# Kernel tuning notes

Measured on AMD Instinct MI355X. Metric: run time of the kernel, lower is better.

## Reference

```python
import jax, jax.numpy as jnp
import numpy as np

N_NODES = 50000
N_EDGES = 800000
IN_DIM = 128
HID = 64
HEADS = 4
OUT = 16
N_GRAPHS = 500
NEG_SLOPE = 0.2


def setup_inputs() -> dict:
    key = jax.random.key(0)
    ks = jax.random.split(key, 12)
    x = jax.random.normal(ks[0], (N_NODES, IN_DIM), dtype=jnp.float32)
    edge_index = jax.random.randint(ks[1], (2, N_EDGES), 0, N_NODES, dtype=jnp.int64)
    batch = jnp.sort(jax.random.randint(ks[2], (N_NODES,), 0, N_GRAPHS, dtype=jnp.int64))
    s1 = 1.0 / np.sqrt(IN_DIM)
    s2 = 1.0 / np.sqrt(HID)
    W1 = jax.random.normal(ks[3], (IN_DIM, HEADS * HID), dtype=jnp.float32) * s1
    a1_src = jax.random.normal(ks[4], (HEADS, HID), dtype=jnp.float32) * s2
    a1_dst = jax.random.normal(ks[5], (HEADS, HID), dtype=jnp.float32) * s2
    b1 = jnp.zeros((HID,), dtype=jnp.float32)
    W2 = jax.random.normal(ks[6], (HID, HEADS * HID), dtype=jnp.float32) * s2
    a2_src = jax.random.normal(ks[7], (HEADS, HID), dtype=jnp.float32) * s2
    a2_dst = jax.random.normal(ks[8], (HEADS, HID), dtype=jnp.float32) * s2
    b2 = jnp.zeros((HID,), dtype=jnp.float32)
    fcW = jax.random.normal(ks[9], (HID, OUT), dtype=jnp.float32) * s2
    fcb = jnp.zeros((OUT,), dtype=jnp.float32)
    return {"x": x, "edge_index": edge_index, "batch": batch,
            "W1": W1, "a1_src": a1_src, "a1_dst": a1_dst, "b1": b1,
            "W2": W2, "a2_src": a2_src, "a2_dst": a2_dst, "b2": b2,
            "fcW": fcW, "fcb": fcb}


def gat_conv(x, W, a_src, a_dst, b, src, dst):
    # PyG GATConv with concat=False: per-head linear, edge softmax over dst, head-mean.
    n = x.shape[0]
    h = (x @ W).reshape(n, HEADS, HID)          # [N,H,D]
    alpha_s = jnp.sum(h * a_src, axis=-1)        # [N,H]
    alpha_d = jnp.sum(h * a_dst, axis=-1)        # [N,H]
    e = jax.nn.leaky_relu(alpha_s[src] + alpha_d[dst], NEG_SLOPE)  # [E,H]
    emax = jax.ops.segment_max(e, dst, num_segments=n)
    ex = jnp.exp(e - emax[dst])
    denom = jax.ops.segment_sum(ex, dst, num_segments=n)
    alpha = ex / denom[dst]                      # [E,H], edge softmax per dst
    msg = h[src] * alpha[:, :, None]             # [E,H,D]
    out = jax.ops.segment_sum(msg, dst, num_segments=n)  # [N,H,D]
    return out.mean(axis=1) + b                  # concat=False -> head mean


def reference(x, edge_index, batch, W1, a1_src, a1_dst, b1, W2, a2_src, a2_dst, b2, fcW, fcb):
    n = x.shape[0]
    # PyG GATConv default add_self_loops=True
    loops = jnp.arange(n, dtype=edge_index.dtype)
    src = jnp.concatenate([edge_index[0], loops])
    dst = jnp.concatenate([edge_index[1], loops])
    h = jax.nn.relu(gat_conv(x, W1, a1_src, a1_dst, b1, src, dst))
    h = jax.nn.relu(gat_conv(h, W2, a2_src, a2_dst, b2, src, dst))
    # global_mean_pool over batch ids
    sums = jax.ops.segment_sum(h, batch, num_segments=N_GRAPHS)
    counts = jax.ops.segment_sum(jnp.ones((n,), dtype=h.dtype), batch, num_segments=N_GRAPHS)
    pooled = sums / jnp.clip(counts, 1.0)[:, None]
    return pooled @ fcW + fcb
```

## Files before the change

### kernel.cpp

```cpp
#include <hip/hip_runtime.h>
#include <hip/hip_bf16.h>
#include <hip/hip_fp16.h>

#define NN 50000
#define EE 800000
#define ETOT 850000
#define NG 500
#define NBLK ((NN + 255) / 256)
#define EB ((ETOT + 255) / 256)

typedef __attribute__((ext_vector_type(8))) short bf16x8;
typedef __attribute__((ext_vector_type(4))) float f32x4;
typedef _Float16 h2f __attribute__((ext_vector_type(2)));

__device__ __forceinline__ h2f as_h2(unsigned u) {
    union { unsigned u; h2f h; } x;
    x.u = u;
    return x.h;
}

__device__ __forceinline__ unsigned short bf16_rne(float v) {
    unsigned u = __float_as_uint(v);
    unsigned r = u + 0x7FFFu + ((u >> 16) & 1u);
    return (unsigned short)(r >> 16);
}

__device__ __forceinline__ int detect_stride(const int* __restrict__ ei,
                                             int tid, int* sflag) {
    if (tid < 64) {
        unsigned long long b = __ballot(ei[2 * tid + 1] != 0);
        if (tid == 0) *sflag = b ? 1 : 2;
    }
    __syncthreads();
    return *sflag;
}

__device__ __forceinline__ void prepw_one(const float* __restrict__ W,
                                          const float* __restrict__ asrc,
                                          const float* __restrict__ adst,
                                          unsigned short* __restrict__ bhi,
                                          unsigned short* __restrict__ blo,
                                          float* __restrict__ ap,
                                          float* __restrict__ adp,
                                          int K, int t) {
    int j = t / K, k = t - j * K;
    int d = j >> 2, h = j & 3;
    float v = W[k * 256 + h * 64 + d];
    unsigned short hb = bf16_rne(v);
    float hf = __uint_as_float((unsigned)hb << 16);
    bhi[t] = hb;
    blo[t] = bf16_rne(v - hf);
    if (k == 0) { ap[j] = asrc[h * 64 + d]; adp[j] = adst[h * 64 + d]; }
}

__global__ __launch_bounds__(256) void k_prep(
        const int* __restrict__ ei, int* __restrict__ src32,
        int* __restrict__ dst32, int* __restrict__ deg,
        const float* __restrict__ W1, const float* __restrict__ a1s,
        const float* __restrict__ a1d, const float* __restrict__ W2,
        const float* __restrict__ a2s, const float* __restrict__ a2d,
        unsigned short* __restrict__ b1h, unsigned short* __restrict__ b1l,
        unsigned short* __restrict__ b2h, unsigned short* __restrict__ b2l,
        float* __restrict__ ap1, float* __restrict__ adp1,
        float* __restrict__ ap2, float* __restrict__ adp2) {
    int blk = blockIdx.x;
    if (blk >= EB) {
        int g = blk - EB;
        if (g < 128)
            prepw_one(W1, a1s, a1d, b1h, b1l, ap1, adp1, 128, g * 256 + threadIdx.x);
        else
            prepw_one(W2, a2s, a2d, b2h, b2l, ap2, adp2, 64, (g - 128) * 256 + threadIdx.x);
        return;
    }
    __shared__ int sflag;
    int tid = threadIdx.x;
    int st = detect_stride(ei, tid, &sflag);
    int e = blk * 256 + tid;
    if (e >= ETOT) return;
    int s, d;
    if (e < EE) {
        s = ei[(size_t)st * e];
        d = ei[(size_t)st * (EE + e)];
    } else {
        s = d = e - EE;
    }
    src32[e] = s;
    dst32[e] = d;
    atomicAdd(&deg[d], 1);
}

__global__ __launch_bounds__(256) void k_blocksum(const int* __restrict__ deg,
                                                  int* __restrict__ bsum) {
    __shared__ int l[256];
    int gid = blockIdx.x * 256 + threadIdx.x;
    int tid = threadIdx.x;
    l[tid] = (gid < NN) ? deg[gid] : 0;
    __syncthreads();
    for (int o = 128; o > 0; o >>= 1) {
        if (tid < o) l[tid] += l[tid + o];
        __syncthreads();
    }
    if (tid == 0) bsum[blockIdx.x] = l[0];
}

__global__ __launch_bounds__(256) void k_scan_final(const int* __restrict__ deg,
                                                    const int* __restrict__ bsum,
                                                    int* __restrict__ rowptr,
                                                    int* __restrict__ cursor) {
    __shared__ int lb[256];
    __shared__ int l[256];
    int tid = threadIdx.x;
    int vb = (tid < NBLK) ? bsum[tid] : 0;
    lb[tid] = vb;
    __syncthreads();
    for (int d = 1; d < 256; d <<= 1) {
        int t = (tid >= d) ? lb[tid - d] : 0;
        __syncthreads();
        lb[tid] += t;
        __syncthreads();
    }
    int boffb = lb[blockIdx.x] - bsum[blockIdx.x];
    int gid = blockIdx.x * 256 + tid;
    int v = (gid < NN) ? deg[gid] : 0;
    l[tid] = v;
    __syncthreads();
    for (int d = 1; d < 256; d <<= 1) {
        int t = (tid >= d) ? l[tid - d] : 0;
        __syncthreads();
        l[tid] += t;
        __syncthreads();
    }
    int ex = l[tid] - v + boffb;
    if (gid < NN) { rowptr[gid] = ex; cursor[gid] = ex; }
    if (gid == 0) rowptr[NN] = ETOT;
}

__global__ __launch_bounds__(256) void k_scatter(const int* __restrict__ src32,
                                                 const int* __restrict__ dst32,
                                                 int* __restrict__ cursor,
                                                 int* __restrict__ csr_src) {
    int e = blockIdx.x * 256 + threadIdx.x;
    if (e >= ETOT) return;
    int pos = atomicAdd(&cursor[dst32[e]], 1);
    csr_src[pos] = src32[e];
}

template <int K>
__global__ __launch_bounds__(64) void k_gemm_mfma(
        const float* __restrict__ A,
        const unsigned short* __restrict__ Bhi,
        const unsigned short* __restrict__ Blo,
        const float* __restrict__ aperm,
        const float* __restrict__ adperm,
        __half* __restrict__ C16,
        float* __restrict__ os,
        float* __restrict__ od, int M) {
    const int NC = K / 32;
    int lane = threadIdx.x;
    int l = lane & 15, q = lane >> 4;
    int m0 = blockIdx.x * 32;

    bf16x8 ahi[2][NC], alo[2][NC];
#pragma unroll
    for (int t = 0; t < 2; ++t) {
        int row = m0 + t * 16 + l;
        if (row >= M) row = M - 1;
        const float* arow = A + (size_t)row * K + q * 8;
#pragma unroll
        for (int c = 0; c < NC; ++c) {
            float4 v0 = *(const float4*)(arow + c * 32);
            float4 v1 = *(const float4*)(arow + c * 32 + 4);
            float vv[8] = {v0.x, v0.y, v0.z, v0.w, v1.x, v1.y, v1.z, v1.w};
#pragma unroll
            for (int j = 0; j < 8; ++j) {
                unsigned short hb = bf16_rne(vv[j]);
                float hf = __uint_as_float((unsigned)hb << 16);
                ahi[t][c][j] = (short)hb;
                alo[t][c][j] = (short)bf16_rne(vv[j] - hf);
            }
        }
    }

    float ps[2][4] = {}, pd[2][4] = {};
    const size_t brow = (size_t)l * K + q * 8;
#pragma unroll 2
    for (int n = 0; n < 16; ++n) {
        const unsigned short* bh = Bhi + (size_t)(n * 16) * K + brow;
        const unsigned short* bl = Blo + (size_t)(n * 16) * K + brow;
        bf16x8 bhf[NC], blf[NC];
#pragma unroll
        for (int c = 0; c < NC; ++c) {
            bhf[c] = *(const bf16x8*)(bh + c * 32);
            blf[c] = *(const bf16x8*)(bl + c * 32);
        }
        f32x4 acc0 = {0.f, 0.f, 0.f, 0.f}, acc1 = {0.f, 0.f, 0.f, 0.f};
#pragma unroll
        for (int c = 0; c < NC; ++c) {
            acc0 = __builtin_amdgcn_mfma_f32_16x16x32_bf16(ahi[0][c], bhf[c], acc0, 0, 0, 0);
            acc1 = __builtin_amdgcn_mfma_f32_16x16x32_bf16(ahi[1][c], bhf[c], acc1, 0, 0, 0);
            acc0 = __builtin_amdgcn_mfma_f32_16x16x32_bf16(ahi[0][c], blf[c], acc0, 0, 0, 0);
            acc1 = __builtin_amdgcn_mfma_f32_16x16x32_bf16(ahi[1][c], blf[c], acc1, 0, 0, 0);
            acc0 = __builtin_amdgcn_mfma_f32_16x16x32_bf16(alo[0][c], bhf[c], acc0, 0, 0, 0);
            acc1 = __builtin_amdgcn_mfma_f32_16x16x32_bf16(alo[1][c], bhf[c], acc1, 0, 0, 0);
        }
        float av = aperm[n * 16 + l], dv = adperm[n * 16 + l];
#pragma unroll
        for (int r = 0; r < 4; ++r) {
            ps[0][r] += acc0[r] * av; pd[0][r] += acc0[r] * dv;
            ps[1][r] += acc1[r] * av; pd[1][r] += acc1[r] * dv;
            int gm0 = m0 + q * 4 + r;
            if (gm0 < M) C16[(size_t)gm0 * 256 + n * 16 + l] = __float2half(acc0[r]);
            int gm1 = m0 + 16 + q * 4 + r;
            if (gm1 < M) C16[(size_t)gm1 * 256 + n * 16 + l] = __float2half(acc1[r]);
        }
    }
#pragma unroll
    for (int t = 0; t < 2; ++t)
#pragma unroll
        for (int r = 0; r < 4; ++r) {
            ps[t][r] += __shfl_xor(ps[t][r], 4);
            ps[t][r] += __shfl_xor(ps[t][r], 8);
            pd[t][r] += __shfl_xor(pd[t][r], 4);
            pd[t][r] += __shfl_xor(pd[t][r], 8);
        }
    if (l < 4) {
#pragma unroll
        for (int t = 0; t < 2; ++t)
#pragma unroll
            for (int r = 0; r < 4; ++r) {
                int gm = m0 + t * 16 + q * 4 + r;
                if (gm < M) {
                    os[(size_t)gm * 4 + l] = ps[t][r];
                    od[(size_t)gm * 4 + l] = pd[t][r];
                }
            }
    }
}

__device__ __forceinline__ float lrelu_exp(float x) {
    x = x > 0.f ? x : 0.2f * x;
    return __expf(x);
}

__global__ __launch_bounds__(256) void k_aggr(const int* __restrict__ rowptr,
                                              const int* __restrict__ csr_src,
                                              const float* __restrict__ as_,
                                              const float* __restrict__ ad_,
                                              const __half* __restrict__ h16,
                                              const float* __restrict__ bias,
                                              float* __restrict__ out) {
    __shared__ uint2 als16[4][64];
    __shared__ int sss[4][64];
    int w = threadIdx.x >> 6;
    int lane = threadIdx.x & 63;
    int d = blockIdx.x * 4 + w;
    if (d >= NN) return;
    int beg = rowptr[d], end = rowptr[d + 1];
    float4 adv = *(const float4*)(ad_ + d * 4);

    int s0 = 0;
    float4 u0 = make_float4(0.f, 0.f, 0.f, 0.f);
    float4 den = make_float4(0.f, 0.f, 0.f, 0.f);
    int i0 = beg + lane;
    if (i0 < end) {
        s0 = csr_src[i0];
        float4 sv = *(const float4*)(as_ + s0 * 4);
        u0.x = lrelu_exp(sv.x + adv.x);
        u0.y = lrelu_exp(sv.y + adv.y);
        u0.z = lrelu_exp(sv.z + adv.z);
        u0.w = lrelu_exp(sv.w + adv.w);
        den = u0;
    }
    for (int i = i0 + 64; i < end; i += 64) {
        int s = csr_src[i];
        float4 sv = *(const float4*)(as_ + s * 4);
        den.x += lrelu_exp(sv.x + adv.x);
        den.y += lrelu_exp(sv.y + adv.y);
        den.z += lrelu_exp(sv.z + adv.z);
        den.w += lrelu_exp(sv.w + adv.w);
    }
#pragma unroll
    for (int off = 32; off > 0; off >>= 1) {
        den.x += __shfl_xor(den.x, off);
        den.y += __shfl_xor(den.y, off);
        den.z += __shfl_xor(den.z, off);
        den.w += __shfl_xor(den.w, off);
    }
    float4 dinv = make_float4(0.25f / den.x, 0.25f / den.y,
                              0.25f / den.z, 0.25f / den.w);
    {
        __half2 q0 = __floats2half2_rn(u0.x * dinv.x, u0.y * dinv.y);
        __half2 q1 = __floats2half2_rn(u0.z * dinv.z, u0.w * dinv.w);
        als16[w][lane] = make_uint2(*(unsigned*)&q0, *(unsigned*)&q1);
        sss[w][lane] = s0;
    }

    int cnt = end - beg;
    if (cnt > 64) cnt = 64;
    int cnt4 = (cnt + 3) & ~3;
    float acc = 0.f;
    int4 sq = *(const int4*)&sss[w][0];
    uint2 r0 = *(const uint2*)(h16 + (size_t)sq.x * 256 + lane * 4);
    uint2 r1 = *(const uint2*)(h16 + (size_t)sq.y * 256 + lane * 4);
    uint2 r2 = *(const uint2*)(h16 + (size_t)sq.z * 256 + lane * 4);
    uint2 r3 = *(const uint2*)(h16 + (size_t)sq.w * 256 + lane * 4);
    for (int j = 0; j < cnt4; j += 4) {
        int jn = (j + 4) & 63;
        int4 sn = *(const int4*)&sss[w][jn];
        uint2 n0 = *(const uint2*)(h16 + (size_t)sn.x * 256 + lane * 4);
        uint2 n1 = *(const uint2*)(h16 + (size_t)sn.y * 256 + lane * 4);
        uint2 n2 = *(const uint2*)(h16 + (size_t)sn.z * 256 + lane * 4);
        uint2 n3 = *(const uint2*)(h16 + (size_t)sn.w * 256 + lane * 4);
        uint4 A01 = *(const uint4*)&als16[w][j];
        uint4 A23 = *(const uint4*)&als16[w][j + 2];
        acc = __builtin_amdgcn_fdot2(as_h2(r0.x), as_h2(A01.x), acc, false);
        acc = __builtin_amdgcn_fdot2(as_h2(r0.y), as_h2(A01.y), acc, false);
        acc = __builtin_amdgcn_fdot2(as_h2(r1.x), as_h2(A01.z), acc, false);
        acc = __builtin_amdgcn_fdot2(as_h2(r1.y), as_h2(A01.w), acc, false);
        acc = __builtin_amdgcn_fdot2(as_h2(r2.x), as_h2(A23.x), acc, false);
        acc = __builtin_amdgcn_fdot2(as_h2(r2.y), as_h2(A23.y), acc, false);
        acc = __builtin_amdgcn_fdot2(as_h2(r3.x), as_h2(A23.z), acc, false);
        acc = __builtin_amdgcn_fdot2(as_h2(r3.y), as_h2(A23.w), acc, false);
        r0 = n0; r1 = n1; r2 = n2; r3 = n3;
    }
    for (int chunk = beg + 64; chunk < end; chunk += 64) {
        int i = chunk + lane;
        int s = 0;
        float4 al = make_float4(0.f, 0.f, 0.f, 0.f);
        if (i < end) {
            s = csr_src[i];
            float4 sv = *(const float4*)(as_ + s * 4);
            al.x = lrelu_exp(sv.x + adv.x) * dinv.x;
            al.y = lrelu_exp(sv.y + adv.y) * dinv.y;
            al.z = lrelu_exp(sv.z + adv.z) * dinv.z;
            al.w = lrelu_exp(sv.w + adv.w) * dinv.w;
        }
        int cc = end - chunk;
        if (cc > 64) cc = 64;
        for (int j = 0; j < cc; ++j) {
            int sj = __shfl(s, j);
            float a0 = __shfl(al.x, j), a1 = __shfl(al.y, j);
            float a2 = __shfl(al.z, j), a3 = __shfl(al.w, j);
            uint2 raw = *(const uint2*)(h16 + (size_t)sj * 256 + lane * 4);
            float2 fa = __half22float2(*(const __half2*)&raw.x);
            float2 fb = __half22float2(*(const __half2*)&raw.y);
            acc += a0 * fa.x + a1 * fa.y + a2 * fb.x + a3 * fb.y;
        }
    }
    float v = acc + bias[lane];
    out[d * 64 + lane] = v > 0.f ? v : 0.f;
}

__global__ __launch_bounds__(256) void k_pool_fc(const float* __restrict__ x3,
                                                 const int* __restrict__ batch,
                                                 const int* __restrict__ ei,
                                                 const float* __restrict__ fcW,
                                                 const float* __restrict__ fcb,
                                                 float* __restrict__ out) {
    __shared__ int sflag;
    int tid = threadIdx.x, lane = tid & 63, w = tid >> 6;
    int st = detect_stride(ei, tid, &sflag);
    int g = blockIdx.x;
    int lo = 0, hi = NN;
    while (lo < hi) { int mid = (lo + hi) >> 1; if (batch[(size_t)st * mid] < g) lo = mid + 1; else hi = mid; }
    int start = lo;
    hi = NN;
    while (lo < hi) { int mid = (lo + hi) >> 1; if (batch[(size_t)st * mid] < g + 1) lo = mid + 1; else hi = mid; }
    int end = lo;
    float sum = 0.f;
    for (int n = start + w; n < end; n += 4) sum += x3[n * 64 + lane];
    __shared__ float ls[4][64];
    ls[w][lane] = sum;
    __syncthreads();
    if (w == 0) {
        float c = (float)(end - start);
        if (c < 1.f) c = 1.f;
        float p = (ls[0][lane] + ls[1][lane] + ls[2][lane] + ls[3][lane]) / c;
#pragma unroll
        for (int o = 0; o < 16; ++o) {
            float v = p * fcW[lane * 16 + o];
#pragma unroll
            for (int off = 32; off > 0; off >>= 1) v += __shfl_down(v, off);
            if (lane == 0) out[g * 16 + o] = v + fcb[o];
        }
    }
}

extern "C" void kernel_launch(void* const* d_in, const int* in_sizes, int n_in,
                              void* d_out, int out_size, void* d_ws, size_t ws_size,
                              hipStream_t stream) {
    const float* x   = (const float*)d_in[0];
    const int*   ei  = (const int*)d_in[1];
    const int*   bat = (const int*)d_in[2];
    const float* W1  = (const float*)d_in[3];
    const float* a1s = (const float*)d_in[4];
    const float* a1d = (const float*)d_in[5];
    const float* b1  = (const float*)d_in[6];
    const float* W2  = (const float*)d_in[7];
    const float* a2s = (const float*)d_in[8];
    const float* a2d = (const float*)d_in[9];
    const float* b2  = (const float*)d_in[10];
    const float* fcW = (const float*)d_in[11];
    const float* fcb = (const float*)d_in[12];
    float* out = (float*)d_out;

    float* ws = (float*)d_ws;
    __half* h16  = (__half*)(ws + 256);
    float* as_   = (float*)(h16 + (size_t)NN * 256);
    float* ad_   = as_ + NN * 4;
    float* xacc  = ad_ + NN * 4;
    int* src32   = (int*)(xacc + (size_t)NN * 64);
    int* dst32   = src32 + ETOT;
    int* deg     = dst32 + ETOT;
    int* rowptr  = deg + NN;
    int* cursor  = rowptr + NN + 1;
    int* csr_src = cursor + NN;
    int* bsum    = csr_src + ETOT;
    char* p = (char*)(bsum + NBLK);
    p = (char*)(((size_t)p + 255) & ~(size_t)255);
    unsigned short* bt1h = (unsigned short*)p; p += 256 * 128 * 2;
    unsigned short* bt1l = (unsigned short*)p; p += 256 * 128 * 2;
    unsigned short* bt2h = (unsigned short*)p; p += 256 * 64 * 2;
    unsigned short* bt2l = (unsigned short*)p; p += 256 * 64 * 2;
    float* ap1  = (float*)p; p += 256 * 4;
    float* adp1 = (float*)p; p += 256 * 4;
    float* ap2  = (float*)p; p += 256 * 4;
    float* adp2 = (float*)p; p += 256 * 4;

    const int wb = (NN * 64 + 255) / 256;

    hipMemsetAsync(deg, 0, NN * sizeof(int), stream);
    k_prep<<<EB + 192, 256, 0, stream>>>(ei, src32, dst32, deg,
                                         W1, a1s, a1d, W2, a2s, a2d,
                                         bt1h, bt1l, bt2h, bt2l,
                                         ap1, adp1, ap2, adp2);
    k_blocksum<<<NBLK, 256, 0, stream>>>(deg, bsum);
    k_scan_final<<<NBLK, 256, 0, stream>>>(deg, bsum, rowptr, cursor);
    k_scatter<<<EB, 256, 0, stream>>>(src32, dst32, cursor, csr_src);

    const int gg = (NN + 31) / 32;
    k_gemm_mfma<128><<<gg, 64, 0, stream>>>(x, bt1h, bt1l, ap1, adp1, h16, as_, ad_, NN);
    k_aggr<<<wb, 256, 0, stream>>>(rowptr, csr_src, as_, ad_, h16, b1, xacc);
    k_gemm_mfma<64><<<gg, 64, 0, stream>>>(xacc, bt2h, bt2l, ap2, adp2, h16, as_, ad_, NN);
    k_aggr<<<wb, 256, 0, stream>>>(rowptr, csr_src, as_, ad_, h16, b2, xacc);
    k_pool_fc<<<NG, 256, 0, stream>>>(xacc, bat, ei, fcW, fcb, out);
}
```

Before: 379.1 us.

## Split GEMM N across two blocks, fuse mean-pool into second aggregation

```diff
diff --git a/kernel.cpp b/kernel.cpp
--- a/kernel.cpp
+++ b/kernel.cpp
@@ -54,8 +54,9 @@
 }
 
 __global__ __launch_bounds__(256) void k_prep(
-        const int* __restrict__ ei, int* __restrict__ src32,
-        int* __restrict__ dst32, int* __restrict__ deg,
+        const int* __restrict__ ei, const int* __restrict__ batch,
+        int* __restrict__ src32, int* __restrict__ dst32,
+        int* __restrict__ deg, int* __restrict__ bat32,
         const float* __restrict__ W1, const float* __restrict__ a1s,
         const float* __restrict__ a1d, const float* __restrict__ W2,
         const float* __restrict__ a2s, const float* __restrict__ a2d,
@@ -64,17 +65,22 @@
         float* __restrict__ ap1, float* __restrict__ adp1,
         float* __restrict__ ap2, float* __restrict__ adp2) {
     int blk = blockIdx.x;
-    if (blk >= EB) {
+    int tid = threadIdx.x;
+    if (blk >= EB && blk < EB + 192) {
         int g = blk - EB;
         if (g < 128)
-            prepw_one(W1, a1s, a1d, b1h, b1l, ap1, adp1, 128, g * 256 + threadIdx.x);
+            prepw_one(W1, a1s, a1d, b1h, b1l, ap1, adp1, 128, g * 256 + tid);
         else
-            prepw_one(W2, a2s, a2d, b2h, b2l, ap2, adp2, 64, (g - 128) * 256 + threadIdx.x);
+            prepw_one(W2, a2s, a2d, b2h, b2l, ap2, adp2, 64, (g - 128) * 256 + tid);
         return;
     }
     __shared__ int sflag;
-    int tid = threadIdx.x;
     int st = detect_stride(ei, tid, &sflag);
+    if (blk >= EB + 192) {
+        int gid = (blk - EB - 192) * 256 + tid;
+        if (gid < NN) bat32[gid] = batch[(size_t)st * gid];
+        return;
+    }
     int e = blk * 256 + tid;
     if (e >= ETOT) return;
     int s, d;
@@ -158,7 +164,9 @@
     const int NC = K / 32;
     int lane = threadIdx.x;
     int l = lane & 15, q = lane >> 4;
-    int m0 = blockIdx.x * 32;
+    int bid = blockIdx.x;
+    int m0 = (bid >> 1) * 32;
+    int nbeg = (bid & 1) * 8;
 
     bf16x8 ahi[2][NC], alo[2][NC];
 #pragma unroll
@@ -184,7 +192,7 @@
     float ps[2][4] = {}, pd[2][4] = {};
     const size_t brow = (size_t)l * K + q * 8;
 #pragma unroll 2
-    for (int n = 0; n < 16; ++n) {
+    for (int n = nbeg; n < nbeg + 8; ++n) {
         const unsigned short* bh = Bhi + (size_t)(n * 16) * K + brow;
         const unsigned short* bl = Blo + (size_t)(n * 16) * K + brow;
         bf16x8 bhf[NC], blf[NC];
@@ -230,8 +238,8 @@
             for (int r = 0; r < 4; ++r) {
                 int gm = m0 + t * 16 + q * 4 + r;
                 if (gm < M) {
-                    os[(size_t)gm * 4 + l] = ps[t][r];
-                    od[(size_t)gm * 4 + l] = pd[t][r];
+                    atomicAdd(&os[(size_t)gm * 4 + l], ps[t][r]);
+                    atomicAdd(&od[(size_t)gm * 4 + l], pd[t][r]);
                 }
             }
     }
@@ -242,13 +250,16 @@
     return __expf(x);
 }
 
+template <bool POOL>
 __global__ __launch_bounds__(256) void k_aggr(const int* __restrict__ rowptr,
                                               const int* __restrict__ csr_src,
                                               const float* __restrict__ as_,
                                               const float* __restrict__ ad_,
                                               const __half* __restrict__ h16,
                                               const float* __restrict__ bias,
-                                              float* __restrict__ out) {
+                                              float* __restrict__ out,
+                                              const int* __restrict__ bat32,
+                                              float* __restrict__ pool) {
     __shared__ uint2 als16[4][64];
     __shared__ int sss[4][64];
     int w = threadIdx.x >> 6;
@@ -348,41 +359,37 @@
         }
     }
     float v = acc + bias[lane];
-    out[d * 64 + lane] = v > 0.f ? v : 0.f;
-}
-
-__global__ __launch_bounds__(256) void k_pool_fc(const float* __restrict__ x3,
-                                                 const int* __restrict__ batch,
-                                                 const int* __restrict__ ei,
-                                                 const float* __restrict__ fcW,
-                                                 const float* __restrict__ fcb,
-                                                 float* __restrict__ out) {
-    __shared__ int sflag;
-    int tid = threadIdx.x, lane = tid & 63, w = tid >> 6;
-    int st = detect_stride(ei, tid, &sflag);
+    v = v > 0.f ? v : 0.f;
+    if (POOL) {
+        int g = bat32[d];
+        atomicAdd(&pool[(size_t)g * 64 + lane], v);
+    } else {
+        out[(size_t)d * 64 + lane] = v;
+    }
+}
+
+__global__ __launch_bounds__(64) void k_fc(const float* __restrict__ pool,
+                                           const int* __restrict__ bat32,
+                                           const float* __restrict__ fcW,
+                                           const float* __restrict__ fcb,
+                                           float* __restrict__ out) {
     int g = blockIdx.x;
+    int d = threadIdx.x;
     int lo = 0, hi = NN;
-    while (lo < hi) { int mid = (lo + hi) >> 1; if (batch[(size_t)st * mid] < g) lo = mid + 1; else hi = mid; }
+    while (lo < hi) { int mid = (lo + hi) >> 1; if (bat32[mid] < g) lo = mid + 1; else hi = mid; }
     int start = lo;
     hi = NN;
-    while (lo < hi) { int mid = (lo + hi) >> 1; if (batch[(size_t)st * mid] < g + 1) lo = mid + 1; else hi = mid; }
+    while (lo < hi) { int mid = (lo + hi) >> 1; if (bat32[mid] < g + 1) lo = mid + 1; else hi = mid; }
     int end = lo;
-    float sum = 0.f;
-    for (int n = start + w; n < end; n += 4) sum += x3[n * 64 + lane];
-    __shared__ float ls[4][64];
-    ls[w][lane] = sum;
-    __syncthreads();
-    if (w == 0) {
-        float c = (float)(end - start);
-        if (c < 1.f) c = 1.f;
-        float p = (ls[0][lane] + ls[1][lane] + ls[2][lane] + ls[3][lane]) / c;
-#pragma unroll
-        for (int o = 0; o < 16; ++o) {
-            float v = p * fcW[lane * 16 + o];
-#pragma unroll
-            for (int off = 32; off > 0; off >>= 1) v += __shfl_down(v, off);
-            if (lane == 0) out[g * 16 + o] = v + fcb[o];
-        }
+    float c = (float)(end - start);
+    if (c < 1.f) c = 1.f;
+    float p = pool[(size_t)g * 64 + d] / c;
+#pragma unroll
+    for (int o = 0; o < 16; ++o) {
+        float v = p * fcW[d * 16 + o];
+#pragma unroll
+        for (int off = 32; off > 0; off >>= 1) v += __shfl_down(v, off);
+        if (d == 0) out[g * 16 + o] = v + fcb[o];
     }
 }
 
@@ -406,13 +413,15 @@
 
     float* ws = (float*)d_ws;
     __half* h16  = (__half*)(ws + 256);
-    float* as_   = (float*)(h16 + (size_t)NN * 256);
-    float* ad_   = as_ + NN * 4;
-    float* xacc  = ad_ + NN * 4;
+    int*   deg  = (int*)(h16 + (size_t)NN * 256);
+    float* as_  = (float*)(deg + NN);
+    float* ad_  = as_ + NN * 4;
+    float* pool = ad_ + NN * 4;
+    float* xacc = pool + NG * 64;
     int* src32   = (int*)(xacc + (size_t)NN * 64);
     int* dst32   = src32 + ETOT;
-    int* deg     = dst32 + ETOT;
-    int* rowptr  = deg + NN;
+    int* bat32   = dst32 + ETOT;
+    int* rowptr  = bat32 + NN;
     int* cursor  = rowptr + NN + 1;
     int* csr_src = cursor + NN;
     int* bsum    = csr_src + ETOT;
@@ -429,19 +438,22 @@
 
     const int wb = (NN * 64 + 255) / 256;
 
-    hipMemsetAsync(deg, 0, NN * sizeof(int), stream);
-    k_prep<<<EB + 192, 256, 0, stream>>>(ei, src32, dst32, deg,
-                                         W1, a1s, a1d, W2, a2s, a2d,
-                                         bt1h, bt1l, bt2h, bt2l,
-                                         ap1, adp1, ap2, adp2);
+    hipMemsetAsync(deg, 0, (size_t)(NN * 9 + NG * 64) * 4, stream);
+    k_prep<<<EB + 192 + NBLK, 256, 0, stream>>>(
+        ei, bat, src32, dst32, deg, bat32,
+        W1, a1s, a1d, W2, a2s, a2d,
+        bt1h, bt1l, bt2h, bt2l, ap1, adp1, ap2, adp2);
     k_blocksum<<<NBLK, 256, 0, stream>>>(deg, bsum);
     k_scan_final<<<NBLK, 256, 0, stream>>>(deg, bsum, rowptr, cursor);
     k_scatter<<<EB, 256, 0, stream>>>(src32, dst32, cursor, csr_src);
 
-    const int gg = (NN + 31) / 32;
+    const int gg = ((NN + 31) / 32) * 2;
     k_gemm_mfma<128><<<gg, 64, 0, stream>>>(x, bt1h, bt1l, ap1, adp1, h16, as_, ad_, NN);
-    k_aggr<<<wb, 256, 0, stream>>>(rowptr, csr_src, as_, ad_, h16, b1, xacc);
+    k_aggr<false><<<wb, 256, 0, stream>>>(rowptr, csr_src, as_, ad_, h16, b1,
+                                          xacc, bat32, pool);
+    hipMemsetAsync(as_, 0, (size_t)NN * 8 * 4, stream);
     k_gemm_mfma<64><<<gg, 64, 0, stream>>>(xacc, bt2h, bt2l, ap2, adp2, h16, as_, ad_, NN);
-    k_aggr<<<wb, 256, 0, stream>>>(rowptr, csr_src, as_, ad_, h16, b2, xacc);
-    k_pool_fc<<<NG, 256, 0, stream>>>(xacc, bat, ei, fcW, fcb, out);
-}
+    k_aggr<true><<<wb, 256, 0, stream>>>(rowptr, csr_src, as_, ad_, h16, b2,
+                                         nullptr, bat32, pool);
+    k_fc<<<NG, 64, 0, stream>>>(pool, bat32, fcW, fcb, out);
+}
```

Result: slower. 390.0 us (+2.9%).

## Swap MFMA operand roles in GEMM for vectorized row-contiguous fp16 stores

Applied to the files above, without the earlier changes.

```diff
diff --git a/kernel.cpp b/kernel.cpp
--- a/kernel.cpp
+++ b/kernel.cpp
@@ -154,18 +154,15 @@
         const float* __restrict__ adperm,
         __half* __restrict__ C16,
         float* __restrict__ os,
-        float* __restrict__ od, int M) {
+        float* __restrict__ od) {
     const int NC = K / 32;
     int lane = threadIdx.x;
     int l = lane & 15, q = lane >> 4;
-    int m0 = blockIdx.x * 32;
-
-    bf16x8 ahi[2][NC], alo[2][NC];
-#pragma unroll
-    for (int t = 0; t < 2; ++t) {
-        int row = m0 + t * 16 + l;
-        if (row >= M) row = M - 1;
-        const float* arow = A + (size_t)row * K + q * 8;
+    int m0 = blockIdx.x * 16;
+
+    bf16x8 yhi[NC], ylo[NC];
+    {
+        const float* arow = A + (size_t)(m0 + l) * K + q * 8;
 #pragma unroll
         for (int c = 0; c < NC; ++c) {
             float4 v0 = *(const float4*)(arow + c * 32);
@@ -175,65 +172,64 @@
             for (int j = 0; j < 8; ++j) {
                 unsigned short hb = bf16_rne(vv[j]);
                 float hf = __uint_as_float((unsigned)hb << 16);
-                ahi[t][c][j] = (short)hb;
-                alo[t][c][j] = (short)bf16_rne(vv[j] - hf);
+                yhi[c][j] = (short)hb;
+                ylo[c][j] = (short)bf16_rne(vv[j] - hf);
             }
         }
     }
 
-    float ps[2][4] = {}, pd[2][4] = {};
-    const size_t brow = (size_t)l * K + q * 8;
-#pragma unroll 2
-    for (int n = 0; n < 16; ++n) {
-        const unsigned short* bh = Bhi + (size_t)(n * 16) * K + brow;
-        const unsigned short* bl = Blo + (size_t)(n * 16) * K + brow;
-        bf16x8 bhf[NC], blf[NC];
+    float ps[4] = {}, pd[4] = {};
+    const size_t brow0 = (size_t)l * K + q * 8;
+#pragma unroll
+    for (int nt = 0; nt < 16; nt += 2) {
+        const unsigned short* bh0 = Bhi + (size_t)(nt * 16) * K + brow0;
+        const unsigned short* bl0 = Blo + (size_t)(nt * 16) * K + brow0;
+        const unsigned short* bh1 = bh0 + (size_t)16 * K;
+        const unsigned short* bl1 = bl0 + (size_t)16 * K;
+        bf16x8 xh0[NC], xl0[NC], xh1[NC], xl1[NC];
 #pragma unroll
         for (int c = 0; c < NC; ++c) {
-            bhf[c] = *(const bf16x8*)(bh + c * 32);
-            blf[c] = *(const bf16x8*)(bl + c * 32);
+            xh0[c] = *(const bf16x8*)(bh0 + c * 32);
+            xl0[c] = *(const bf16x8*)(bl0 + c * 32);
+            xh1[c] = *(const bf16x8*)(bh1 + c * 32);
+            xl1[c] = *(const bf16x8*)(bl1 + c * 32);
         }
         f32x4 acc0 = {0.f, 0.f, 0.f, 0.f}, acc1 = {0.f, 0.f, 0.f, 0.f};
 #pragma unroll
         for (int c = 0; c < NC; ++c) {
-            acc0 = __builtin_amdgcn_mfma_f32_16x16x32_bf16(ahi[0][c], bhf[c], acc0, 0, 0, 0);
-            acc1 = __builtin_amdgcn_mfma_f32_16x16x32_bf16(ahi[1][c], bhf[c], acc1, 0, 0, 0);
-            acc0 = __builtin_amdgcn_mfma_f32_16x16x32_bf16(ahi[0][c], blf[c], acc0, 0, 0, 0);
-            acc1 = __builtin_amdgcn_mfma_f32_16x16x32_bf16(ahi[1][c], blf[c], acc1, 0, 0, 0);
-            acc0 = __builtin_amdgcn_mfma_f32_16x16x32_bf16(alo[0][c], bhf[c], acc0, 0, 0, 0);
-            acc1 = __builtin_amdgcn_mfma_f32_16x16x32_bf16(alo[1][c], bhf[c], acc1, 0, 0, 0);
-        }
-        float av = aperm[n * 16 + l], dv = adperm[n * 16 + l];
-#pragma unroll
-        for (int r = 0; r < 4; ++r) {
-            ps[0][r] += acc0[r] * av; pd[0][r] += acc0[r] * dv;
-            ps[1][r] += acc1[r] * av; pd[1][r] += acc1[r] * dv;
-            int gm0 = m0 + q * 4 + r;
-            if (gm0 < M) C16[(size_t)gm0 * 256 + n * 16 + l] = __float2half(acc0[r]);
-            int gm1 = m0 + 16 + q * 4 + r;
-            if (gm1 < M) C16[(size_t)gm1 * 256 + n * 16 + l] = __float2half(acc1[r]);
-        }
-    }
-#pragma unroll
-    for (int t = 0; t < 2; ++t)
-#pragma unroll
-        for (int r = 0; r < 4; ++r) {
-            ps[t][r] += __shfl_xor(ps[t][r], 4);
-            ps[t][r] += __shfl_xor(ps[t][r], 8);
-            pd[t][r] += __shfl_xor(pd[t][r], 4);
-            pd[t][r] += __shfl_xor(pd[t][r], 8);
-        }
-    if (l < 4) {
-#pragma unroll
-        for (int t = 0; t < 2; ++t)
-#pragma unroll
-            for (int r = 0; r < 4; ++r) {
-                int gm = m0 + t * 16 + q * 4 + r;
-                if (gm < M) {
-                    os[(size_t)gm * 4 + l] = ps[t][r];
-                    od[(size_t)gm * 4 + l] = pd[t][r];
-                }
-            }
+            acc0 = __builtin_amdgcn_mfma_f32_16x16x32_bf16(xh0[c], yhi[c], acc0, 0, 0, 0);
+            acc1 = __builtin_amdgcn_mfma_f32_16x16x32_bf16(xh1[c], yhi[c], acc1, 0, 0, 0);
+            acc0 = __builtin_amdgcn_mfma_f32_16x16x32_bf16(xl0[c], yhi[c], acc0, 0, 0, 0);
+            acc1 = __builtin_amdgcn_mfma_f32_16x16x32_bf16(xl1[c], yhi[c], acc1, 0, 0, 0);
+            acc0 = __builtin_amdgcn_mfma_f32_16x16x32_bf16(xh0[c], ylo[c], acc0, 0, 0, 0);
+            acc1 = __builtin_amdgcn_mfma_f32_16x16x32_bf16(xh1[c], ylo[c], acc1, 0, 0, 0);
+        }
+#pragma unroll
+        for (int t = 0; t < 2; ++t) {
+            f32x4 acc = t ? acc1 : acc0;
+            int n0 = (nt + t) * 16 + q * 4;
+            float4 av = *(const float4*)(aperm + n0);
+            float4 dv = *(const float4*)(adperm + n0);
+            ps[0] += acc[0] * av.x; pd[0] += acc[0] * dv.x;
+            ps[1] += acc[1] * av.y; pd[1] += acc[1] * dv.y;
+            ps[2] += acc[2] * av.z; pd[2] += acc[2] * dv.z;
+            ps[3] += acc[3] * av.w; pd[3] += acc[3] * dv.w;
+            __half2 p0 = __floats2half2_rn(acc[0], acc[1]);
+            __half2 p1 = __floats2half2_rn(acc[2], acc[3]);
+            uint2 pk = make_uint2(*(unsigned*)&p0, *(unsigned*)&p1);
+            *(uint2*)(C16 + (size_t)(m0 + l) * 256 + n0) = pk;
+        }
+    }
+#pragma unroll
+    for (int r = 0; r < 4; ++r) {
+        ps[r] += __shfl_xor(ps[r], 16);
+        ps[r] += __shfl_xor(ps[r], 32);
+        pd[r] += __shfl_xor(pd[r], 16);
+        pd[r] += __shfl_xor(pd[r], 32);
+    }
+    if (lane < 16) {
+        *(float4*)(os + (size_t)(m0 + l) * 4) = make_float4(ps[0], ps[1], ps[2], ps[3]);
+        *(float4*)(od + (size_t)(m0 + l) * 4) = make_float4(pd[0], pd[1], pd[2], pd[3]);
     }
 }
 
@@ -438,10 +434,10 @@
     k_scan_final<<<NBLK, 256, 0, stream>>>(deg, bsum, rowptr, cursor);
     k_scatter<<<EB, 256, 0, stream>>>(src32, dst32, cursor, csr_src);
 
-    const int gg = (NN + 31) / 32;
-    k_gemm_mfma<128><<<gg, 64, 0, stream>>>(x, bt1h, bt1l, ap1, adp1, h16, as_, ad_, NN);
+    const int gg = NN / 16;
+    k_gemm_mfma<128><<<gg, 64, 0, stream>>>(x, bt1h, bt1l, ap1, adp1, h16, as_, ad_);
     k_aggr<<<wb, 256, 0, stream>>>(rowptr, csr_src, as_, ad_, h16, b1, xacc);
-    k_gemm_mfma<64><<<gg, 64, 0, stream>>>(xacc, bt2h, bt2l, ap2, adp2, h16, as_, ad_, NN);
+    k_gemm_mfma<64><<<gg, 64, 0, stream>>>(xacc, bt2h, bt2l, ap2, adp2, h16, as_, ad_);
     k_aggr<<<wb, 256, 0, stream>>>(rowptr, csr_src, as_, ad_, h16, b2, xacc);
     k_pool_fc<<<NG, 256, 0, stream>>>(xacc, bat, ei, fcW, fcb, out);
 }
```

Result: slower. 420.0 us (+10.8%).
